# Optimization experiments

Hardware: AMD Instinct MI355X
Metric: run time of the kernel (lower is better)

## Reference

```python
import jax, jax.numpy as jnp
import numpy as np

N_NODES = 100000
N_EDGES = 1600000
IN_F = 128
OUT_F = 64


def setup_inputs() -> dict:
    key = jax.random.key(0)
    k1, k2, k3, k4, k5, k6 = jax.random.split(key, 6)
    stdv = 1.0 / np.sqrt(OUT_F)
    return {
        "input": jax.random.normal(k1, (N_NODES, IN_F), dtype=jnp.float32),
        "weights": jax.random.uniform(k2, (IN_F, OUT_F), minval=-stdv, maxval=stdv, dtype=jnp.float32),
        "bias": jax.random.uniform(k3, (OUT_F,), minval=-stdv, maxval=stdv, dtype=jnp.float32),
        "adj_vals": jax.random.uniform(k4, (N_EDGES,), dtype=jnp.float32),
        "adj_rows": jax.random.randint(k5, (N_EDGES,), 0, N_NODES, dtype=jnp.int32),
        "adj_cols": jax.random.randint(k6, (N_EDGES,), 0, N_NODES, dtype=jnp.int32),
    }


def reference(input, weights, bias, adj_vals, adj_rows, adj_cols):
    # Dense transform: support = input @ W   -> [N, out_features]
    support = jnp.matmul(input, weights)
    # Sparse adjacency matmul (COO SpMM): out[r] += v * support[c]
    msgs = adj_vals[:, None] * support[adj_cols]          # [E, out_features]
    output = jax.ops.segment_sum(msgs, adj_rows, num_segments=N_NODES)
    # Fused bias epilogue
    return output + bias
```

## Files before the change

kernel.cpp:

```cpp
#include <hip/hip_runtime.h>
#include <hip/hip_bf16.h>

#define N_NODES 100000
#define IN_F 128
#define OUT_F 64
#define BROWS 64
#define NB 1563
#define BIN_TILE 4096
#define CSB_CAP 2048
#define ASTRIDE 132

__device__ __forceinline__ unsigned short f2bf(float x) {
    unsigned u = __float_as_uint(x);
    u += 0x7FFFu + ((u >> 16) & 1u);
    return (unsigned short)(u >> 16);
}
__device__ __forceinline__ float bf2f(unsigned short s) {
    return __uint_as_float(((unsigned)s) << 16);
}

__global__ __launch_bounds__(256) void count_kernel(
    const int* __restrict__ rows, int* __restrict__ cnt, int nE)
{
    __shared__ int hist[NB];
    const int t = threadIdx.x;
    for (int i = t; i < NB; i += 256) hist[i] = 0;
    __syncthreads();

    for (int e = blockIdx.x * 256 + t; e < nE; e += gridDim.x * 256)
        atomicAdd(&hist[rows[e] >> 6], 1);
    __syncthreads();

    for (int i = t; i < NB; i += 256) {
        int h = hist[i];
        if (h) atomicAdd(&cnt[i], h);
    }
}

__global__ __launch_bounds__(256) void scan_kernel(
    const int* __restrict__ cnt, int* __restrict__ base,
    int* __restrict__ cursor, int nE)
{
    __shared__ int lds[256];
    const int t = threadIdx.x;
    const int i0 = t * 8;
    int c[8];
    int tot = 0;
    #pragma unroll
    for (int k = 0; k < 8; ++k) {
        c[k] = (i0 + k < NB) ? cnt[i0 + k] : 0;
        tot += c[k];
    }

    lds[t] = tot;
    __syncthreads();
    int sum = tot;
    #pragma unroll
    for (int off = 1; off < 256; off <<= 1) {
        int y = (t >= off) ? lds[t - off] : 0;
        __syncthreads();
        sum += y;
        lds[t] = sum;
        __syncthreads();
    }
    int run = sum - tot;

    #pragma unroll
    for (int k = 0; k < 8; ++k) {
        if (i0 + k < NB) { base[i0 + k] = run; cursor[i0 + k] = run; }
        run += c[k];
    }
    if (t == 0) base[NB] = nE;
}

__global__ __launch_bounds__(256) void gemm_bin_kernel(
    const float* __restrict__ in, const float* __restrict__ W,
    unsigned short* __restrict__ support,
    const int* __restrict__ rows, const int* __restrict__ cols,
    const float* __restrict__ vals, int* __restrict__ cursor,
    uint2* __restrict__ binned, int nE, int gemmBlocks)
{
    __shared__ __align__(16) char smem[64 * ASTRIDE * 4];
    const int t = threadIdx.x;

    if ((int)blockIdx.x >= gemmBlocks) {
        int* hist  = (int*)smem;
        int* lbase = hist + NB;
        const int tb = (blockIdx.x - gemmBlocks) * BIN_TILE;

        for (int i = t; i < NB; i += 256) hist[i] = 0;
        __syncthreads();

        int myr[16], myrank[16];
        #pragma unroll
        for (int i = 0; i < 16; ++i) {
            int e = tb + i * 256 + t;
            if (e < nE) {
                int r = rows[e];
                myr[i] = r;
                myrank[i] = atomicAdd(&hist[r >> 6], 1);
            } else myr[i] = -1;
        }
        __syncthreads();

        for (int i = t; i < NB; i += 256) {
            int h = hist[i];
            lbase[i] = h ? atomicAdd(&cursor[i], h) : 0;
        }
        __syncthreads();

        #pragma unroll
        for (int i = 0; i < 16; ++i) {
            int e = tb + i * 256 + t;
            if (e < nE) {
                int r = myr[i];
                unsigned pack = ((unsigned)(r & (BROWS - 1)) << 17)
                              | (unsigned)cols[e];
                binned[lbase[r >> 6] + myrank[i]] =
                    make_uint2(pack, __float_as_uint(vals[e]));
            }
        }
        return;
    }

    float* Alds = (float*)smem;
    const long row0 = (long)blockIdx.x * 64;

    #pragma unroll
    for (int i = 0; i < 8; ++i) {
        int fi = t + i * 256;
        int r  = fi >> 5;
        int c4 = (fi & 31) << 2;
        float4 v = make_float4(0.f, 0.f, 0.f, 0.f);
        if (row0 + r < N_NODES)
            v = *(const float4*)(in + (row0 + r) * IN_F + c4);
        *(float4*)(Alds + r * ASTRIDE + c4) = v;
    }
    __syncthreads();

    const int lane = t & 63;
    const int c0   = __builtin_amdgcn_readfirstlane((t >> 6) << 4);
    const float* __restrict__ Wp = W + c0;

    float acc[16];
    #pragma unroll
    for (int i = 0; i < 16; ++i) acc[i] = 0.f;

    const float* Ar = Alds + lane * ASTRIDE;
    #pragma unroll 4
    for (int k4 = 0; k4 < IN_F; k4 += 4) {
        const float4 av = *(const float4*)(Ar + k4);
        #pragma unroll
        for (int j = 0; j < 4; ++j) {
            const float a = (j == 0) ? av.x : (j == 1) ? av.y
                           : (j == 2) ? av.z : av.w;
            const int k = k4 + j;
            const float4 w0 = *(const float4*)(Wp + k * OUT_F + 0);
            const float4 w1 = *(const float4*)(Wp + k * OUT_F + 4);
            const float4 w2 = *(const float4*)(Wp + k * OUT_F + 8);
            const float4 w3 = *(const float4*)(Wp + k * OUT_F + 12);
            acc[0]  = fmaf(a, w0.x, acc[0]);  acc[1]  = fmaf(a, w0.y, acc[1]);
            acc[2]  = fmaf(a, w0.z, acc[2]);  acc[3]  = fmaf(a, w0.w, acc[3]);
            acc[4]  = fmaf(a, w1.x, acc[4]);  acc[5]  = fmaf(a, w1.y, acc[5]);
            acc[6]  = fmaf(a, w1.z, acc[6]);  acc[7]  = fmaf(a, w1.w, acc[7]);
            acc[8]  = fmaf(a, w2.x, acc[8]);  acc[9]  = fmaf(a, w2.y, acc[9]);
            acc[10] = fmaf(a, w2.z, acc[10]); acc[11] = fmaf(a, w2.w, acc[11]);
            acc[12] = fmaf(a, w3.x, acc[12]); acc[13] = fmaf(a, w3.y, acc[13]);
            acc[14] = fmaf(a, w3.z, acc[14]); acc[15] = fmaf(a, w3.w, acc[15]);
        }
    }

    const long orow = row0 + lane;
    if (orow < N_NODES) {
        unsigned up[8];
        #pragma unroll
        for (int i = 0; i < 8; ++i)
            up[i] = (unsigned)f2bf(acc[2 * i]) |
                    ((unsigned)f2bf(acc[2 * i + 1]) << 16);
        unsigned short* o = support + orow * OUT_F + c0;
        *(uint4*)(o + 0) = make_uint4(up[0], up[1], up[2], up[3]);
        *(uint4*)(o + 8) = make_uint4(up[4], up[5], up[6], up[7]);
    }
}

__global__ __launch_bounds__(1024, 2) void csr_spmm(
    const int* __restrict__ base, const uint2* __restrict__ binned,
    const unsigned short* __restrict__ support, const float* __restrict__ bias,
    float* __restrict__ out)
{
    __shared__ uint2 stage[CSB_CAP];
    __shared__ uint2 sorted[CSB_CAP];
    __shared__ int rh[BROWS], rs[BROWS + 1], rc[BROWS];
    const int t = threadIdx.x;
    const int b = blockIdx.x;
    const int s = base[b], e = base[b + 1];
    const int n = e - s;
    const int wid  = t >> 6;
    const int lane = t & 63;
    const int row0 = b * BROWS;

    if (t < BROWS) rh[t] = 0;
    __syncthreads();

    if (n <= CSB_CAP) {
        for (int i = t; i < n; i += 1024) {
            uint2 p = binned[s + i];
            stage[i] = p;
            atomicAdd(&rh[p.x >> 17], 1);
        }
        __syncthreads();
        if (t < BROWS) {
            int v = rh[t];
            int inc = v;
            #pragma unroll
            for (int off = 1; off < BROWS; off <<= 1) {
                int y = __shfl_up(inc, off, 64);
                if (t >= off) inc += y;
            }
            rs[t] = inc - v;
            rc[t] = inc - v;
            if (t == BROWS - 1) rs[BROWS] = inc;
        }
        __syncthreads();
        for (int i = t; i < n; i += 1024) {
            uint2 p = stage[i];
            int pos = atomicAdd(&rc[p.x >> 17], 1);
            sorted[pos] = p;
        }
        __syncthreads();

        #pragma unroll
        for (int q = 0; q < 4; ++q) {
            const int rr = wid * 4 + q;
            const int r  = row0 + rr;
            if (r >= N_NODES) break;
            float acc = bias[lane];
            int j  = rs[rr];
            const int je = rs[rr + 1];
            for (; j + 7 < je; j += 8) {
                uint2 q0 = sorted[j + 0];
                uint2 q1 = sorted[j + 1];
                uint2 q2 = sorted[j + 2];
                uint2 q3 = sorted[j + 3];
                uint2 q4 = sorted[j + 4];
                uint2 q5 = sorted[j + 5];
                uint2 q6 = sorted[j + 6];
                uint2 q7 = sorted[j + 7];
                float g0 = bf2f(support[((size_t)(q0.x & 131071u) << 6) + lane]);
                float g1 = bf2f(support[((size_t)(q1.x & 131071u) << 6) + lane]);
                float g2 = bf2f(support[((size_t)(q2.x & 131071u) << 6) + lane]);
                float g3 = bf2f(support[((size_t)(q3.x & 131071u) << 6) + lane]);
                float g4 = bf2f(support[((size_t)(q4.x & 131071u) << 6) + lane]);
                float g5 = bf2f(support[((size_t)(q5.x & 131071u) << 6) + lane]);
                float g6 = bf2f(support[((size_t)(q6.x & 131071u) << 6) + lane]);
                float g7 = bf2f(support[((size_t)(q7.x & 131071u) << 6) + lane]);
                acc = fmaf(__uint_as_float(q0.y), g0, acc);
                acc = fmaf(__uint_as_float(q1.y), g1, acc);
                acc = fmaf(__uint_as_float(q2.y), g2, acc);
                acc = fmaf(__uint_as_float(q3.y), g3, acc);
                acc = fmaf(__uint_as_float(q4.y), g4, acc);
                acc = fmaf(__uint_as_float(q5.y), g5, acc);
                acc = fmaf(__uint_as_float(q6.y), g6, acc);
                acc = fmaf(__uint_as_float(q7.y), g7, acc);
            }
            for (; j < je; ++j) {
                uint2 p = sorted[j];
                acc = fmaf(__uint_as_float(p.y),
                           bf2f(support[((size_t)(p.x & 131071u) << 6) + lane]),
                           acc);
            }
            out[(size_t)r * OUT_F + lane] = acc;
        }
    } else {
        #pragma unroll
        for (int q = 0; q < 4; ++q) {
            const int rr = wid * 4 + q;
            const int r  = row0 + rr;
            if (r >= N_NODES) break;
            float acc = bias[lane];
            for (int j = s; j < e; ++j) {
                uint2 p = binned[j];
                if ((int)(p.x >> 17) == rr)
                    acc = fmaf(__uint_as_float(p.y),
                               bf2f(support[((size_t)(p.x & 131071u) << 6) + lane]),
                               acc);
            }
            out[(size_t)r * OUT_F + lane] = acc;
        }
    }
}

__global__ __launch_bounds__(256) void bias_init_kernel(
    float* __restrict__ out, const float* __restrict__ bias, int total4)
{
    const float4* b4 = (const float4*)bias;
    float4* o4 = (float4*)out;
    int i = blockIdx.x * blockDim.x + threadIdx.x;
    int stride = gridDim.x * blockDim.x;
    for (; i < total4; i += stride)
        o4[i] = b4[i & 15];
}

__global__ __launch_bounds__(256) void scatter_kernel(
    const float* __restrict__ vals, const int* __restrict__ rows,
    const int* __restrict__ cols, const unsigned short* __restrict__ support,
    float* __restrict__ out, int nE)
{
    const int e = blockIdx.x * 4 + (threadIdx.x >> 6);
    if (e >= nE) return;
    const int f = threadIdx.x & 63;
    const float m = vals[e] * bf2f(support[(size_t)cols[e] * OUT_F + f]);
    atomicAdd(&out[(size_t)rows[e] * OUT_F + f], m);
}

extern "C" void kernel_launch(void* const* d_in, const int* in_sizes, int n_in,
                              void* d_out, int out_size, void* d_ws, size_t ws_size,
                              hipStream_t stream) {
    const float* input    = (const float*)d_in[0];
    const float* weights  = (const float*)d_in[1];
    const float* bias     = (const float*)d_in[2];
    const float* adj_vals = (const float*)d_in[3];
    const int*   adj_rows = (const int*)d_in[4];
    const int*   adj_cols = (const int*)d_in[5];
    const int nE = in_sizes[3];

    float* out = (float*)d_out;
    const int gemmBlocks = (N_NODES + 63) / 64;
    const int binBlocks  = (nE + BIN_TILE - 1) / BIN_TILE;

    char* ws = (char*)d_ws;
    const size_t off_support = 0;
    const size_t off_base    = 12800000;
    const size_t off_cursor  = off_base + 6400;
    const size_t off_binned  = off_cursor + 6400;
    const size_t required    = off_binned + (size_t)nE * 8;

    unsigned short* support = (unsigned short*)(ws + off_support);
    int*   bbase   = (int*)  (ws + off_base);
    int*   cursor  = (int*)  (ws + off_cursor);
    uint2* binned  = (uint2*)(ws + off_binned);

    if (ws_size >= required) {
        hipMemsetAsync(cursor, 0, NB * sizeof(int), stream);
        hipLaunchKernelGGL(count_kernel, dim3(256), dim3(256), 0, stream,
                           adj_rows, cursor, nE);
        hipLaunchKernelGGL(scan_kernel, dim3(1), dim3(256), 0, stream,
                           cursor, bbase, cursor, nE);
        hipLaunchKernelGGL(gemm_bin_kernel, dim3(gemmBlocks + binBlocks),
                           dim3(256), 0, stream,
                           input, weights, support,
                           adj_rows, adj_cols, adj_vals, cursor, binned,
                           nE, gemmBlocks);
        hipLaunchKernelGGL(csr_spmm, dim3(NB), dim3(1024), 0, stream,
                           bbase, binned, support, bias, out);
    } else {
        hipLaunchKernelGGL(gemm_bin_kernel, dim3(gemmBlocks), dim3(256),
                           0, stream, input, weights, support,
                           adj_rows, adj_cols, adj_vals, (int*)nullptr,
                           (uint2*)nullptr, nE, gemmBlocks);
        hipLaunchKernelGGL(bias_init_kernel, dim3(2048), dim3(256), 0, stream,
                           out, bias, N_NODES * OUT_F / 4);
        hipLaunchKernelGGL(scatter_kernel, dim3((nE + 3) / 4), dim3(256),
                           0, stream, adj_vals, adj_rows, adj_cols, support,
                           out, nE);
    }
}
```

Before: 130.5 us.

## Split fused GEMM/binning kernel and hold W columns in registers

Measured after the change: 157.9 us. 1.21x slower.

```diff
diff --git a/kernel.cpp b/kernel.cpp
--- a/kernel.cpp
+++ b/kernel.cpp
@@ -8,7 +8,6 @@
 #define NB 1563
 #define BIN_TILE 4096
 #define CSB_CAP 2048
-#define ASTRIDE 132
 
 __device__ __forceinline__ unsigned short f2bf(float x) {
     unsigned u = __float_as_uint(x);
@@ -19,111 +18,12 @@
     return __uint_as_float(((unsigned)s) << 16);
 }
 
-__global__ __launch_bounds__(256) void count_kernel(
-    const int* __restrict__ rows, int* __restrict__ cnt, int nE)
-{
-    __shared__ int hist[NB];
+__global__ __launch_bounds__(256, 3) void gemm_kernel(
+    const float* __restrict__ in, const float* __restrict__ W,
+    unsigned short* __restrict__ support)
+{
+    __shared__ float Alds[64 * IN_F];
     const int t = threadIdx.x;
-    for (int i = t; i < NB; i += 256) hist[i] = 0;
-    __syncthreads();
-
-    for (int e = blockIdx.x * 256 + t; e < nE; e += gridDim.x * 256)
-        atomicAdd(&hist[rows[e] >> 6], 1);
-    __syncthreads();
-
-    for (int i = t; i < NB; i += 256) {
-        int h = hist[i];
-        if (h) atomicAdd(&cnt[i], h);
-    }
-}
-
-__global__ __launch_bounds__(256) void scan_kernel(
-    const int* __restrict__ cnt, int* __restrict__ base,
-    int* __restrict__ cursor, int nE)
-{
-    __shared__ int lds[256];
-    const int t = threadIdx.x;
-    const int i0 = t * 8;
-    int c[8];
-    int tot = 0;
-    #pragma unroll
-    for (int k = 0; k < 8; ++k) {
-        c[k] = (i0 + k < NB) ? cnt[i0 + k] : 0;
-        tot += c[k];
-    }
-
-    lds[t] = tot;
-    __syncthreads();
-    int sum = tot;
-    #pragma unroll
-    for (int off = 1; off < 256; off <<= 1) {
-        int y = (t >= off) ? lds[t - off] : 0;
-        __syncthreads();
-        sum += y;
-        lds[t] = sum;
-        __syncthreads();
-    }
-    int run = sum - tot;
-
-    #pragma unroll
-    for (int k = 0; k < 8; ++k) {
-        if (i0 + k < NB) { base[i0 + k] = run; cursor[i0 + k] = run; }
-        run += c[k];
-    }
-    if (t == 0) base[NB] = nE;
-}
-
-__global__ __launch_bounds__(256) void gemm_bin_kernel(
-    const float* __restrict__ in, const float* __restrict__ W,
-    unsigned short* __restrict__ support,
-    const int* __restrict__ rows, const int* __restrict__ cols,
-    const float* __restrict__ vals, int* __restrict__ cursor,
-    uint2* __restrict__ binned, int nE, int gemmBlocks)
-{
-    __shared__ __align__(16) char smem[64 * ASTRIDE * 4];
-    const int t = threadIdx.x;
-
-    if ((int)blockIdx.x >= gemmBlocks) {
-        int* hist  = (int*)smem;
-        int* lbase = hist + NB;
-        const int tb = (blockIdx.x - gemmBlocks) * BIN_TILE;
-
-        for (int i = t; i < NB; i += 256) hist[i] = 0;
-        __syncthreads();
-
-        int myr[16], myrank[16];
-        #pragma unroll
-        for (int i = 0; i < 16; ++i) {
-            int e = tb + i * 256 + t;
-            if (e < nE) {
-                int r = rows[e];
-                myr[i] = r;
-                myrank[i] = atomicAdd(&hist[r >> 6], 1);
-            } else myr[i] = -1;
-        }
-        __syncthreads();
-
-        for (int i = t; i < NB; i += 256) {
-            int h = hist[i];
-            lbase[i] = h ? atomicAdd(&cursor[i], h) : 0;
-        }
-        __syncthreads();
-
-        #pragma unroll
-        for (int i = 0; i < 16; ++i) {
-            int e = tb + i * 256 + t;
-            if (e < nE) {
-                int r = myr[i];
-                unsigned pack = ((unsigned)(r & (BROWS - 1)) << 17)
-                              | (unsigned)cols[e];
-                binned[lbase[r >> 6] + myrank[i]] =
-                    make_uint2(pack, __float_as_uint(vals[e]));
-            }
-        }
-        return;
-    }
-
-    float* Alds = (float*)smem;
     const long row0 = (long)blockIdx.x * 64;
 
     #pragma unroll
@@ -134,52 +34,130 @@
         float4 v = make_float4(0.f, 0.f, 0.f, 0.f);
         if (row0 + r < N_NODES)
             v = *(const float4*)(in + (row0 + r) * IN_F + c4);
-        *(float4*)(Alds + r * ASTRIDE + c4) = v;
-    }
-    __syncthreads();
+        *(float4*)(Alds + r * IN_F + c4) = v;
+    }
 
     const int lane = t & 63;
-    const int c0   = __builtin_amdgcn_readfirstlane((t >> 6) << 4);
-    const float* __restrict__ Wp = W + c0;
-
-    float acc[16];
-    #pragma unroll
-    for (int i = 0; i < 16; ++i) acc[i] = 0.f;
-
-    const float* Ar = Alds + lane * ASTRIDE;
-    #pragma unroll 4
-    for (int k4 = 0; k4 < IN_F; k4 += 4) {
-        const float4 av = *(const float4*)(Ar + k4);
+    float w[IN_F];
+    #pragma unroll
+    for (int k = 0; k < IN_F; ++k)
+        w[k] = W[k * OUT_F + lane];
+
+    __syncthreads();
+
+    const int wid = t >> 6;
+    for (int q = 0; q < 16; ++q) {
+        const int r = wid * 16 + q;
+        const long orow = row0 + r;
+        float acc0 = 0.f, acc1 = 0.f, acc2 = 0.f, acc3 = 0.f;
+        const float4* Ar = (const float4*)(Alds + r * IN_F);
         #pragma unroll
-        for (int j = 0; j < 4; ++j) {
-            const float a = (j == 0) ? av.x : (j == 1) ? av.y
-                           : (j == 2) ? av.z : av.w;
-            const int k = k4 + j;
-            const float4 w0 = *(const float4*)(Wp + k * OUT_F + 0);
-            const float4 w1 = *(const float4*)(Wp + k * OUT_F + 4);
-            const float4 w2 = *(const float4*)(Wp + k * OUT_F + 8);
-            const float4 w3 = *(const float4*)(Wp + k * OUT_F + 12);
-            acc[0]  = fmaf(a, w0.x, acc[0]);  acc[1]  = fmaf(a, w0.y, acc[1]);
-            acc[2]  = fmaf(a, w0.z, acc[2]);  acc[3]  = fmaf(a, w0.w, acc[3]);
-            acc[4]  = fmaf(a, w1.x, acc[4]);  acc[5]  = fmaf(a, w1.y, acc[5]);
-            acc[6]  = fmaf(a, w1.z, acc[6]);  acc[7]  = fmaf(a, w1.w, acc[7]);
-            acc[8]  = fmaf(a, w2.x, acc[8]);  acc[9]  = fmaf(a, w2.y, acc[9]);
-            acc[10] = fmaf(a, w2.z, acc[10]); acc[11] = fmaf(a, w2.w, acc[11]);
-            acc[12] = fmaf(a, w3.x, acc[12]); acc[13] = fmaf(a, w3.y, acc[13]);
-            acc[14] = fmaf(a, w3.z, acc[14]); acc[15] = fmaf(a, w3.w, acc[15]);
-        }
-    }
-
-    const long orow = row0 + lane;
-    if (orow < N_NODES) {
-        unsigned up[8];
-        #pragma unroll
-        for (int i = 0; i < 8; ++i)
-            up[i] = (unsigned)f2bf(acc[2 * i]) |
-                    ((unsigned)f2bf(acc[2 * i + 1]) << 16);
-        unsigned short* o = support + orow * OUT_F + c0;
-        *(uint4*)(o + 0) = make_uint4(up[0], up[1], up[2], up[3]);
-        *(uint4*)(o + 8) = make_uint4(up[4], up[5], up[6], up[7]);
+        for (int i = 0; i < 32; ++i) {
+            const float4 a = Ar[i];
+            acc0 = fmaf(a.x, w[4 * i + 0], acc0);
+            acc1 = fmaf(a.y, w[4 * i + 1], acc1);
+            acc2 = fmaf(a.z, w[4 * i + 2], acc2);
+            acc3 = fmaf(a.w, w[4 * i + 3], acc3);
+        }
+        if (orow < N_NODES)
+            support[orow * OUT_F + lane] = f2bf((acc0 + acc1) + (acc2 + acc3));
+    }
+}
+
+__global__ __launch_bounds__(256) void count_kernel(
+    const int* __restrict__ rows, int* __restrict__ cnt, int nE)
+{
+    __shared__ int hist[NB];
+    const int t = threadIdx.x;
+    for (int i = t; i < NB; i += 256) hist[i] = 0;
+    __syncthreads();
+
+    for (int e = blockIdx.x * 256 + t; e < nE; e += gridDim.x * 256)
+        atomicAdd(&hist[rows[e] >> 6], 1);
+    __syncthreads();
+
+    for (int i = t; i < NB; i += 256) {
+        int h = hist[i];
+        if (h) atomicAdd(&cnt[i], h);
+    }
+}
+
+__global__ __launch_bounds__(256) void scan_kernel(
+    const int* __restrict__ cnt, int* __restrict__ base,
+    int* __restrict__ cursor, int nE)
+{
+    __shared__ int lds[256];
+    const int t = threadIdx.x;
+    const int i0 = t * 8;
+    int c[8];
+    int tot = 0;
+    #pragma unroll
+    for (int k = 0; k < 8; ++k) {
+        c[k] = (i0 + k < NB) ? cnt[i0 + k] : 0;
+        tot += c[k];
+    }
+
+    lds[t] = tot;
+    __syncthreads();
+    int sum = tot;
+    #pragma unroll
+    for (int off = 1; off < 256; off <<= 1) {
+        int y = (t >= off) ? lds[t - off] : 0;
+        __syncthreads();
+        sum += y;
+        lds[t] = sum;
+        __syncthreads();
+    }
+    int run = sum - tot;
+
+    #pragma unroll
+    for (int k = 0; k < 8; ++k) {
+        if (i0 + k < NB) { base[i0 + k] = run; cursor[i0 + k] = run; }
+        run += c[k];
+    }
+    if (t == 0) base[NB] = nE;
+}
+
+__global__ __launch_bounds__(256) void bin_kernel(
+    const int* __restrict__ rows, const int* __restrict__ cols,
+    const float* __restrict__ vals, int* __restrict__ cursor,
+    uint2* __restrict__ binned, int nE)
+{
+    __shared__ int hist[NB];
+    __shared__ int lbase[NB];
+    const int t  = threadIdx.x;
+    const int tb = blockIdx.x * BIN_TILE;
+
+    for (int i = t; i < NB; i += 256) hist[i] = 0;
+    __syncthreads();
+
+    int myr[16], myrank[16];
+    #pragma unroll
+    for (int i = 0; i < 16; ++i) {
+        int e = tb + i * 256 + t;
+        if (e < nE) {
+            int r = rows[e];
+            myr[i] = r;
+            myrank[i] = atomicAdd(&hist[r >> 6], 1);
+        } else myr[i] = -1;
+    }
+    __syncthreads();
+
+    for (int i = t; i < NB; i += 256) {
+        int h = hist[i];
+        lbase[i] = h ? atomicAdd(&cursor[i], h) : 0;
+    }
+    __syncthreads();
+
+    #pragma unroll
+    for (int i = 0; i < 16; ++i) {
+        int e = tb + i * 256 + t;
+        if (e < nE) {
+            int r = myr[i];
+            unsigned pack = ((unsigned)(r & (BROWS - 1)) << 17) | (unsigned)cols[e];
+            binned[lbase[r >> 6] + myrank[i]] =
+                make_uint2(pack, __float_as_uint(vals[e]));
+        }
     }
 }
 
@@ -346,18 +324,15 @@
                            adj_rows, cursor, nE);
         hipLaunchKernelGGL(scan_kernel, dim3(1), dim3(256), 0, stream,
                            cursor, bbase, cursor, nE);
-        hipLaunchKernelGGL(gemm_bin_kernel, dim3(gemmBlocks + binBlocks),
-                           dim3(256), 0, stream,
-                           input, weights, support,
-                           adj_rows, adj_cols, adj_vals, cursor, binned,
-                           nE, gemmBlocks);
+        hipLaunchKernelGGL(gemm_kernel, dim3(gemmBlocks), dim3(256), 0, stream,
+                           input, weights, support);
+        hipLaunchKernelGGL(bin_kernel, dim3(binBlocks), dim3(256), 0, stream,
+                           adj_rows, adj_cols, adj_vals, cursor, binned, nE);
         hipLaunchKernelGGL(csr_spmm, dim3(NB), dim3(1024), 0, stream,
                            bbase, binned, support, bias, out);
     } else {
-        hipLaunchKernelGGL(gemm_bin_kernel, dim3(gemmBlocks), dim3(256),
-                           0, stream, input, weights, support,
-                           adj_rows, adj_cols, adj_vals, (int*)nullptr,
-                           (uint2*)nullptr, nE, gemmBlocks);
+        hipLaunchKernelGGL(gemm_kernel, dim3(gemmBlocks), dim3(256), 0, stream,
+                           input, weights, support);
         hipLaunchKernelGGL(bias_init_kernel, dim3(2048), dim3(256), 0, stream,
                            out, bias, N_NODES * OUT_F / 4);
         hipLaunchKernelGGL(scatter_kernel, dim3((nE + 3) / 4), dim3(256),
```
